# Kernel optimization log

Hardware: AMD Instinct MI355X
Metric: run time of the kernel (lower is better)

## Reference

```python
import jax, jax.numpy as jnp
import numpy as np

P = 16          # patch_size
IMG = 224       # image_size
NP = IMG // P   # 14 patches per side
TOTAL = NP * NP # 196
D = P * P * 3   # 768 features per patch


def setup_inputs() -> dict:
    key = jax.random.key(0)
    k1, k2, k3 = jax.random.split(key, 3)
    B = 256
    x = jax.random.normal(k1, (B, 3, IMG, IMG), dtype=jnp.float32)
    # Stacked per-patch Linear(768, 1) weights/biases (196 unshared extractors).
    weight = jax.random.normal(k2, (TOTAL, D), dtype=jnp.float32) * (1.0 / np.sqrt(D))
    bias = jax.random.normal(k3, (TOTAL,), dtype=jnp.float32) * 0.01
    return {"x": x, "weight": weight, "bias": bias}


def _extract_patches(x):
    # Faithful replication of torch: unfold(2,P,P).unfold(3,P,P) ->
    # [B,C,nH,nW,P,P]; permute(0,4,5,1,2,3) -> [B,P,P,C,nH,nW];
    # contiguous().view(B, 196, C, P, P)  (note: this view scrambles axes,
    # as in the original module; we replicate the exact reinterpretation).
    B, C, H, W = x.shape
    nH, nW = H // P, W // P
    p = x.reshape(B, C, nH, P, nW, P).transpose(0, 1, 2, 4, 3, 5)  # [B,C,nH,nW,P,P]
    p = p.transpose(0, 4, 5, 1, 2, 3)                               # [B,P,P,C,nH,nW]
    return p.reshape(B, TOTAL, D)                                   # flatten per 'patch'


def reference(x, weight, bias):
    patches = _extract_patches(x)                   # [B, 196, 768]
    # 196 unshared Linear(768,1) projections as one batched dot-product.
    scores = jnp.einsum('bpd,pd->bp', patches, weight) + bias  # [B, 196]
    return scores
```

## Files before the change

kernel.cpp:

```cpp
#include <hip/hip_runtime.h>


#define NPATCH 196
#define NF4IMG 37632
#define BSTR   197

__global__ __launch_bounds__(256) void prep_kernel(
    const float* __restrict__ weight,
    const float* __restrict__ bias,
    float* __restrict__ wlay,
    float* __restrict__ out)
{
    const int bid = blockIdx.x;
    if (bid < 147) {
        const int t4 = bid * 256 + threadIdx.x;
        const float4 wv = ((const float4*)weight)[t4];
        const float wt[4] = {wv.x, wv.y, wv.z, wv.w};
        #pragma unroll
        for (int u = 0; u < 4; ++u) {
            const int t    = 4 * t4 + u;
            const int i    = t / 9408;
            const int rem  = t - i * 9408;
            const int jj   = rem / 588;
            const int rem2 = rem - jj * 588;
            const int c    = rem2 / 196;
            const int rem3 = rem2 - c * 196;
            const int h    = rem3 / 14;
            const int w    = rem3 - h * 14;
            wlay[((c * 14 + h) * 14 + w) * 256 + i * 16 + jj] = wt[u];
        }
    } else {
        const int g4 = (bid - 147) * 256 + threadIdx.x;
        const int g  = 4 * g4;
        float4 o;
        o.x = bias[(g + 0) % NPATCH];
        o.y = bias[(g + 1) % NPATCH];
        o.z = bias[(g + 2) % NPATCH];
        o.w = bias[(g + 3) % NPATCH];
        ((float4*)out)[g4] = o;
    }
}

__global__ __launch_bounds__(448) void run_kernel(
    const float* __restrict__ x,
    const float* __restrict__ wlay,
    float* __restrict__ out)
{
    __shared__ float bins[7 * BSTR];
    const int tid  = threadIdx.x;
    const int b    = blockIdx.x >> 1;
    const int hh   = blockIdx.x & 1;
    const int wv   = tid >> 6;
    const int lane = tid & 63;
    const int i    = lane >> 2;
    const int j4   = lane & 3;
    const int h    = hh * 7 + wv;

    for (int k = tid; k < 7 * BSTR; k += 448) bins[k] = 0.0f;
    __syncthreads();

    float* mybins = bins + wv * BSTR;

    #pragma unroll
    for (int c = 0; c < 3; ++c) {
        const int tile = c * 14 + h;
        const float4* __restrict__ x4 = (const float4*)x + (size_t)b * NF4IMG
                                        + c * 12544 + (16 * h + i) * 56 + j4;
        const float4* __restrict__ w4 = (const float4*)wlay + tile * 896 + i * 4 + j4;

        int p0[4], ws_[4];
        #pragma unroll
        for (int dj = 0; dj < 4; ++dj) {
            const int jj = 4 * j4 + dj;
            const int t0 = i * 9408 + jj * 588 + c * 196 + h * 14;
            p0[dj]  = t0 / 768;
            ws_[dj] = 768 * (p0[dj] + 1) - t0;
        }

        float accA[4] = {0.f, 0.f, 0.f, 0.f};
        float accB[4] = {0.f, 0.f, 0.f, 0.f};
        #pragma unroll
        for (int w = 0; w < 14; ++w) {
            const float4 xv  = x4[4 * w];
            const float4 wv_ = w4[64 * w];
            const float xs[4]  = {xv.x, xv.y, xv.z, xv.w};
            const float wsv[4] = {wv_.x, wv_.y, wv_.z, wv_.w};
            #pragma unroll
            for (int dj = 0; dj < 4; ++dj) {
                const float v   = xs[dj] * wsv[dj];
                const float sel = (w < ws_[dj]) ? 1.0f : 0.0f;
                accA[dj] = fmaf(v, sel, accA[dj]);
                accB[dj] = fmaf(v, 1.0f - sel, accB[dj]);
            }
        }

        #pragma unroll
        for (int dj = 0; dj < 4; ++dj) {
            unsafeAtomicAdd(&mybins[p0[dj]], accA[dj]);
            if (ws_[dj] < 14)
                unsafeAtomicAdd(&mybins[p0[dj] + 1], accB[dj]);
        }
    }
    __syncthreads();

    for (int p = tid; p < NPATCH; p += 448) {
        float s = 0.0f;
        #pragma unroll
        for (int k = 0; k < 7; ++k) s += bins[k * BSTR + p];
        unsafeAtomicAdd(&out[b * NPATCH + p], s);
    }
}

extern "C" void kernel_launch(void* const* d_in, const int* in_sizes, int n_in,
                              void* d_out, int out_size, void* d_ws, size_t ws_size,
                              hipStream_t stream) {
    const float* x      = (const float*)d_in[0];
    const float* weight = (const float*)d_in[1];
    const float* bias   = (const float*)d_in[2];
    float* out          = (float*)d_out;
    float* wlay         = (float*)d_ws;

    prep_kernel<<<196, 256, 0, stream>>>(weight, bias, wlay, out);
    run_kernel<<<512, 448, 0, stream>>>(x, wlay, out);
}
```

Baseline: 35.93 us.

## Remap lanes so each wavefront load covers contiguous 128B row segments

Changes the thread-to-data mapping so 8 lanes cover two consecutive 64-byte patch-row chunks (even and odd w), making each wavefront load of x and weights span fully contiguous rows. The weight layout is permuted to match, so weight loads become one contiguous 1KB block per step. Each thread now runs two i-halves of 7 steps instead of 14 steps over one row, which doubles the shared-memory atomic flushes.

New measurement: 40.81 us. 13.6% more time.

```diff
diff --git a/kernel.cpp b/kernel.cpp
--- a/kernel.cpp
+++ b/kernel.cpp
@@ -27,7 +27,14 @@
             const int rem3 = rem2 - c * 196;
             const int h    = rem3 / 14;
             const int w    = rem3 - h * 14;
-            wlay[((c * 14 + h) * 14 + w) * 256 + i * 16 + jj] = wt[u];
+            const int tile  = c * 14 + h;
+            const int ihalf = i >> 3;
+            const int i2    = i & 7;
+            const int q     = (jj >> 2) + ((w & 1) << 2);
+            const int s     = w >> 1;
+            const int lane  = i2 * 8 + q;
+            const int uu    = jj & 3;
+            wlay[((((tile * 2 + ihalf) * 7 + s) * 64) + lane) * 4 + uu] = wt[u];
         }
     } else {
         const int g4 = (bid - 147) * 256 + threadIdx.x;
@@ -52,8 +59,10 @@
     const int hh   = blockIdx.x & 1;
     const int wv   = tid >> 6;
     const int lane = tid & 63;
-    const int i    = lane >> 2;
-    const int j4   = lane & 3;
+    const int i2   = lane >> 3;
+    const int q    = lane & 7;
+    const int q3   = q & 3;
+    const int wodd = q >> 2;
     const int h    = hh * 7 + wv;
 
     for (int k = tid; k < 7 * BSTR; k += 448) bins[k] = 0.0f;
@@ -64,41 +73,47 @@
     #pragma unroll
     for (int c = 0; c < 3; ++c) {
         const int tile = c * 14 + h;
-        const float4* __restrict__ x4 = (const float4*)x + (size_t)b * NF4IMG
-                                        + c * 12544 + (16 * h + i) * 56 + j4;
-        const float4* __restrict__ w4 = (const float4*)wlay + tile * 896 + i * 4 + j4;
+        #pragma unroll
+        for (int ihalf = 0; ihalf < 2; ++ihalf) {
+            const int i = ihalf * 8 + i2;
+            const float4* __restrict__ x4 = (const float4*)x + (size_t)b * NF4IMG
+                                            + c * 12544 + (16 * h + i) * 56 + q;
+            const float4* __restrict__ w4 = (const float4*)wlay
+                                            + (tile * 2 + ihalf) * 7 * 64 + lane;
 
-        int p0[4], ws_[4];
-        #pragma unroll
-        for (int dj = 0; dj < 4; ++dj) {
-            const int jj = 4 * j4 + dj;
-            const int t0 = i * 9408 + jj * 588 + c * 196 + h * 14;
-            p0[dj]  = t0 / 768;
-            ws_[dj] = 768 * (p0[dj] + 1) - t0;
-        }
+            int p0[4], ws_[4];
+            #pragma unroll
+            for (int u = 0; u < 4; ++u) {
+                const int jj = 4 * q3 + u;
+                const int t0 = i * 9408 + jj * 588 + c * 196 + h * 14;
+                p0[u]  = t0 / 768;
+                ws_[u] = 768 * (p0[u] + 1) - t0;
+            }
 
-        float accA[4] = {0.f, 0.f, 0.f, 0.f};
-        float accB[4] = {0.f, 0.f, 0.f, 0.f};
-        #pragma unroll
-        for (int w = 0; w < 14; ++w) {
-            const float4 xv  = x4[4 * w];
-            const float4 wv_ = w4[64 * w];
-            const float xs[4]  = {xv.x, xv.y, xv.z, xv.w};
-            const float wsv[4] = {wv_.x, wv_.y, wv_.z, wv_.w};
+            float accA[4] = {0.f, 0.f, 0.f, 0.f};
+            float accB[4] = {0.f, 0.f, 0.f, 0.f};
             #pragma unroll
-            for (int dj = 0; dj < 4; ++dj) {
-                const float v   = xs[dj] * wsv[dj];
-                const float sel = (w < ws_[dj]) ? 1.0f : 0.0f;
-                accA[dj] = fmaf(v, sel, accA[dj]);
-                accB[dj] = fmaf(v, 1.0f - sel, accB[dj]);
+            for (int s = 0; s < 7; ++s) {
+                const float4 xv  = x4[8 * s];
+                const float4 wv_ = w4[64 * s];
+                const int w = 2 * s + wodd;
+                const float xs[4]  = {xv.x, xv.y, xv.z, xv.w};
+                const float wsv[4] = {wv_.x, wv_.y, wv_.z, wv_.w};
+                #pragma unroll
+                for (int u = 0; u < 4; ++u) {
+                    const float v   = xs[u] * wsv[u];
+                    const float sel = (w < ws_[u]) ? 1.0f : 0.0f;
+                    accA[u] = fmaf(v, sel, accA[u]);
+                    accB[u] = fmaf(v, 1.0f - sel, accB[u]);
+                }
             }
-        }
 
-        #pragma unroll
-        for (int dj = 0; dj < 4; ++dj) {
-            unsafeAtomicAdd(&mybins[p0[dj]], accA[dj]);
-            if (ws_[dj] < 14)
-                unsafeAtomicAdd(&mybins[p0[dj] + 1], accB[dj]);
+            #pragma unroll
+            for (int u = 0; u < 4; ++u) {
+                unsafeAtomicAdd(&mybins[p0[u]], accA[u]);
+                if (ws_[u] < 14)
+                    unsafeAtomicAdd(&mybins[p0[u] + 1], accB[u]);
+            }
         }
     }
     __syncthreads();
```

## Split run kernel by channel and process two images per block for weight reuse

Applied to the files above, without the earlier changes.

Each block now handles one colour channel for a pair of images instead of all three channels for one image. Every weight load is reused across both images, and the grid grows from 512 to 768 blocks. All waves share two LDS bin rows, which raises contention on the shared atomics. The number of global atomic adds into the output triples, since three channel blocks now contribute to each output.

Result: slower. 40.03 us (+11.4%).

```diff
diff --git a/kernel.cpp b/kernel.cpp
--- a/kernel.cpp
+++ b/kernel.cpp
@@ -46,68 +46,74 @@
     const float* __restrict__ wlay,
     float* __restrict__ out)
 {
-    __shared__ float bins[7 * BSTR];
+    __shared__ float bins[2 * BSTR];
     const int tid  = threadIdx.x;
-    const int b    = blockIdx.x >> 1;
-    const int hh   = blockIdx.x & 1;
+    const int r    = blockIdx.x & 255;
+    const int c    = blockIdx.x >> 8;
+    const int hh   = r & 1;
+    const int b0   = (r >> 1) * 2;
     const int wv   = tid >> 6;
     const int lane = tid & 63;
     const int i    = lane >> 2;
     const int j4   = lane & 3;
     const int h    = hh * 7 + wv;
+    const int tile = c * 14 + h;
 
-    for (int k = tid; k < 7 * BSTR; k += 448) bins[k] = 0.0f;
+    for (int k = tid; k < 2 * BSTR; k += 448) bins[k] = 0.0f;
     __syncthreads();
 
-    float* mybins = bins + wv * BSTR;
+    const float4* __restrict__ x40 = (const float4*)x + (size_t)b0 * NF4IMG
+                                     + c * 12544 + (16 * h + i) * 56 + j4;
+    const float4* __restrict__ x41 = x40 + NF4IMG;
+    const float4* __restrict__ w4  = (const float4*)wlay + tile * 896 + i * 4 + j4;
+
+    int p0[4], ws_[4];
+    #pragma unroll
+    for (int u = 0; u < 4; ++u) {
+        const int jj = 4 * j4 + u;
+        const int t0 = i * 9408 + jj * 588 + c * 196 + h * 14;
+        p0[u]  = t0 / 768;
+        ws_[u] = 768 * (p0[u] + 1) - t0;
+    }
+
+    float accA0[4] = {0.f, 0.f, 0.f, 0.f}, accB0[4] = {0.f, 0.f, 0.f, 0.f};
+    float accA1[4] = {0.f, 0.f, 0.f, 0.f}, accB1[4] = {0.f, 0.f, 0.f, 0.f};
 
     #pragma unroll
-    for (int c = 0; c < 3; ++c) {
-        const int tile = c * 14 + h;
-        const float4* __restrict__ x4 = (const float4*)x + (size_t)b * NF4IMG
-                                        + c * 12544 + (16 * h + i) * 56 + j4;
-        const float4* __restrict__ w4 = (const float4*)wlay + tile * 896 + i * 4 + j4;
+    for (int w = 0; w < 14; ++w) {
+        const float4 wv_ = w4[64 * w];
+        const float4 xv0 = x40[4 * w];
+        const float4 xv1 = x41[4 * w];
+        const float wsv[4] = {wv_.x, wv_.y, wv_.z, wv_.w};
+        const float xs0[4] = {xv0.x, xv0.y, xv0.z, xv0.w};
+        const float xs1[4] = {xv1.x, xv1.y, xv1.z, xv1.w};
+        #pragma unroll
+        for (int u = 0; u < 4; ++u) {
+            const float sel = (w < ws_[u]) ? 1.0f : 0.0f;
+            const float v0  = xs0[u] * wsv[u];
+            const float v1  = xs1[u] * wsv[u];
+            accA0[u] = fmaf(v0, sel, accA0[u]);
+            accB0[u] = fmaf(v0, 1.0f - sel, accB0[u]);
+            accA1[u] = fmaf(v1, sel, accA1[u]);
+            accB1[u] = fmaf(v1, 1.0f - sel, accB1[u]);
+        }
+    }
 
-        int p0[4], ws_[4];
-        #pragma unroll
-        for (int dj = 0; dj < 4; ++dj) {
-            const int jj = 4 * j4 + dj;
-            const int t0 = i * 9408 + jj * 588 + c * 196 + h * 14;
-            p0[dj]  = t0 / 768;
-            ws_[dj] = 768 * (p0[dj] + 1) - t0;
-        }
-
-        float accA[4] = {0.f, 0.f, 0.f, 0.f};
-        float accB[4] = {0.f, 0.f, 0.f, 0.f};
-        #pragma unroll
-        for (int w = 0; w < 14; ++w) {
-            const float4 xv  = x4[4 * w];
-            const float4 wv_ = w4[64 * w];
-            const float xs[4]  = {xv.x, xv.y, xv.z, xv.w};
-            const float wsv[4] = {wv_.x, wv_.y, wv_.z, wv_.w};
-            #pragma unroll
-            for (int dj = 0; dj < 4; ++dj) {
-                const float v   = xs[dj] * wsv[dj];
-                const float sel = (w < ws_[dj]) ? 1.0f : 0.0f;
-                accA[dj] = fmaf(v, sel, accA[dj]);
-                accB[dj] = fmaf(v, 1.0f - sel, accB[dj]);
-            }
-        }
-
-        #pragma unroll
-        for (int dj = 0; dj < 4; ++dj) {
-            unsafeAtomicAdd(&mybins[p0[dj]], accA[dj]);
-            if (ws_[dj] < 14)
-                unsafeAtomicAdd(&mybins[p0[dj] + 1], accB[dj]);
+    #pragma unroll
+    for (int u = 0; u < 4; ++u) {
+        unsafeAtomicAdd(&bins[p0[u]], accA0[u]);
+        unsafeAtomicAdd(&bins[BSTR + p0[u]], accA1[u]);
+        if (ws_[u] < 14) {
+            unsafeAtomicAdd(&bins[p0[u] + 1], accB0[u]);
+            unsafeAtomicAdd(&bins[BSTR + p0[u] + 1], accB1[u]);
         }
     }
     __syncthreads();
 
-    for (int p = tid; p < NPATCH; p += 448) {
-        float s = 0.0f;
-        #pragma unroll
-        for (int k = 0; k < 7; ++k) s += bins[k * BSTR + p];
-        unsafeAtomicAdd(&out[b * NPATCH + p], s);
+    for (int k = tid; k < 2 * NPATCH; k += 448) {
+        const int img = k / NPATCH;
+        const int p   = k - img * NPATCH;
+        unsafeAtomicAdd(&out[(b0 + img) * NPATCH + p], bins[img * BSTR + p]);
     }
 }
 
@@ -121,5 +127,5 @@
     float* wlay         = (float*)d_ws;
 
     prep_kernel<<<196, 256, 0, stream>>>(weight, bias, wlay, out);
-    run_kernel<<<512, 448, 0, stream>>>(x, wlay, out);
+    run_kernel<<<768, 448, 0, stream>>>(x, wlay, out);
 }
```
